# Kernel tuning notes

Measured on AMD Instinct MI355X. Metric: run time of the kernel, lower is better.

Reference implementation:

```python
import jax, jax.numpy as jnp
import numpy as np
import math

B, C, TC, H, W = 8, 256, 512, 48, 48
EPS = 1e-6

def setup_inputs() -> dict:
    key = jax.random.key(0)
    kx, kt, kq, kk, kv = jax.random.split(key, 5)
    x = jax.random.normal(kx, (B, C, H, W), dtype=jnp.float32)
    token = jax.random.normal(kt, (B, TC, H, W), dtype=jnp.float32)
    # xavier_uniform for 1x1 conv weights [out, in]
    def xavier(k, fan_out, fan_in):
        a = math.sqrt(6.0 / (fan_in + fan_out))
        return jax.random.uniform(k, (fan_out, fan_in), dtype=jnp.float32, minval=-a, maxval=a)
    Wq = xavier(kq, C, C)
    Wk = xavier(kk, C, TC)
    Wv = xavier(kv, C, TC)
    alpha = jnp.float32(0.5)  # nonzero so the attention path affects the output
    return {"x": x, "token": token, "Wq": Wq, "Wk": Wk, "Wv": Wv, "alpha": alpha}

def reference(x, token, Wq, Wk, Wv, alpha):
    # 1x1 convs == per-pixel GEMMs over the channel dim
    q = jnp.einsum('oc,bchw->bohw', Wq, x)       # [B,C,H,W]
    k = jnp.einsum('oc,bchw->bohw', Wk, token)   # [B,C,H,W]
    v = jnp.einsum('oc,bchw->bohw', Wv, token)   # [B,C,H,W]
    b, c, h, w = q.shape
    n = h * w
    qf = q.reshape(b, c, n).transpose(0, 2, 1)   # [B,N,C]
    kf = k.reshape(b, c, n)                      # [B,C,N]
    vf = v.reshape(b, c, n).transpose(0, 2, 1)   # [B,N,C]
    # cosine normalization over the channel dim (F.normalize with eps clamp)
    qn = qf / jnp.maximum(jnp.linalg.norm(qf, axis=-1, keepdims=True), EPS)
    kn = kf / jnp.maximum(jnp.linalg.norm(kf, axis=1, keepdims=True), EPS)
    attn = jnp.einsum('bnc,bcm->bnm', qn, kn) / math.sqrt(c)  # [B,N,N]
    attn = jax.nn.softmax(attn, axis=-1)
    out = jnp.einsum('bnm,bmc->bnc', attn, vf)   # [B,N,C]
    out = out.transpose(0, 2, 1).reshape(b, c, h, w)
    return x + alpha * out
```

## Files before the change

kernel.cpp:

```cpp
#include <hip/hip_runtime.h>

#define B_   8
#define C_   256
#define TC_  512
#define HW_  2304
#define EPS_ 1e-6f

typedef __bf16 bf16_t;
typedef __bf16 bf16x8 __attribute__((ext_vector_type(8)));
typedef __bf16 bf16x4_t __attribute__((ext_vector_type(4)));
typedef float  f32x4 __attribute__((ext_vector_type(4)));
typedef unsigned int  u32;
typedef long long     i64;
typedef unsigned char u8;

__device__ __forceinline__ void g2l16(const void* g, void* l) {
    __builtin_amdgcn_global_load_lds(
        (const __attribute__((address_space(1))) unsigned int*)g,
        (__attribute__((address_space(3))) unsigned int*)l, 16, 0, 0);
}

__device__ __forceinline__ u8 to_fp8(float v) {
    return (u8)(__builtin_amdgcn_cvt_pk_fp8_f32(v, v, 0, false) & 0xff);
}

__global__ __launch_bounds__(256)
void wfrag_kernel(const float* __restrict__ wq, const float* __restrict__ wk,
                  const float* __restrict__ wv,
                  bf16_t* __restrict__ oq, bf16_t* __restrict__ ok,
                  bf16_t* __restrict__ ov)
{
    const int fid = blockIdx.x * 4 + (threadIdx.x >> 6);
    const int lane = threadIdx.x & 63;
    const int l16 = lane & 15, quad = lane >> 4;

    const float* src; bf16_t* dst; int cin, f;
    if (fid < 128)      { src = wq; dst = oq; cin = C_;  f = fid; }
    else if (fid < 384) { src = wk; dst = ok; cin = TC_; f = fid - 128; }
    else                { src = wv; dst = ov; cin = TC_; f = fid - 384; }
    const int nks = cin / 32;
    const int ot = f / nks, ks = f % nks;

    const float* s = src + (size_t)(ot * 16 + l16) * cin + ks * 32 + quad * 8;
    float4 a = *(const float4*)(s);
    float4 b = *(const float4*)(s + 4);
    bf16x8 o;
    o[0] = (__bf16)a.x; o[1] = (__bf16)a.y; o[2] = (__bf16)a.z; o[3] = (__bf16)a.w;
    o[4] = (__bf16)b.x; o[5] = (__bf16)b.y; o[6] = (__bf16)b.z; o[7] = (__bf16)b.w;
    *(bf16x8*)(dst + (size_t)f * 512 + lane * 8) = o;
}

template<int CIN, bool DO_V, bool KFMT>
__global__ __launch_bounds__(256, 4)
void convqkv_kernel(const float* __restrict__ X, const bf16_t* __restrict__ Wa,
                    const bf16_t* __restrict__ Wvp, u8* __restrict__ outA,
                    u8* __restrict__ outV)
{
    const int bid = blockIdx.x;
    const int b  = bid & 7;
    const int n0 = (bid >> 3) * 16;
    const int tid = threadIdx.x;
    const int wv = tid >> 6;
    const int lane = tid & 63;
    const int quad = lane >> 4, l16 = lane & 15;
    const int NKS = CIN / 32;

    __shared__ bf16_t T[16][CIN + 8];
    __shared__ float ssp[4][16];

    {
        const float* Xb = X + (size_t)b * CIN * HW_ + n0;
        const int cl = tid >> 2;
        const int n4 = (tid & 3) * 4;
#pragma unroll
        for (int cp = 0; cp < CIN; cp += 64) {
            float4 v = *(const float4*)(Xb + (size_t)(cp + cl) * HW_ + n4);
            T[n4 + 0][cp + cl] = (__bf16)v.x;
            T[n4 + 1][cp + cl] = (__bf16)v.y;
            T[n4 + 2][cp + cl] = (__bf16)v.z;
            T[n4 + 3][cp + cl] = (__bf16)v.w;
        }
    }
    __syncthreads();

    bf16x8 af[CIN / 32];
#pragma unroll
    for (int ks = 0; ks < CIN / 32; ks++)
        af[ks] = *(const bf16x8*)(&T[l16][ks * 32 + quad * 8]);

    const int ot0 = wv * 4;

    f32x4 accK[4];
#pragma unroll
    for (int p = 0; p < 4; p++) accK[p] = (f32x4){0.f, 0.f, 0.f, 0.f};
    {
        const bf16_t* wbase = Wa + ((size_t)ot0 * NKS) * 512 + lane * 8;
#pragma unroll
        for (int ks = 0; ks < CIN / 32; ks++)
#pragma unroll
            for (int p = 0; p < 4; p++) {
                bf16x8 bw = *(const bf16x8*)(wbase + (size_t)(p * NKS + ks) * 512);
                accK[p] = __builtin_amdgcn_mfma_f32_16x16x32_bf16(af[ks], bw, accK[p], 0, 0, 0);
            }
    }

    {
        float ssr[4];
#pragma unroll
        for (int r = 0; r < 4; r++) {
            float ss = accK[0][r] * accK[0][r] + accK[1][r] * accK[1][r]
                     + accK[2][r] * accK[2][r] + accK[3][r] * accK[3][r];
            ss += __shfl_xor(ss, 1);
            ss += __shfl_xor(ss, 2);
            ss += __shfl_xor(ss, 4);
            ss += __shfl_xor(ss, 8);
            ssr[r] = ss;
        }
        if (l16 == 0) {
#pragma unroll
            for (int r = 0; r < 4; r++) ssp[wv][quad * 4 + r] = ssr[r];
        }
    }

    f32x4 accV[4];
    if (DO_V) {
#pragma unroll
        for (int p = 0; p < 4; p++) accV[p] = (f32x4){0.f, 0.f, 0.f, 0.f};
        const bf16_t* wbase = Wvp + ((size_t)ot0 * NKS) * 512 + lane * 8;
#pragma unroll
        for (int ks = 0; ks < CIN / 32; ks++)
#pragma unroll
            for (int p = 0; p < 4; p++) {
                bf16x8 aw = *(const bf16x8*)(wbase + (size_t)(p * NKS + ks) * 512);
                accV[p] = __builtin_amdgcn_mfma_f32_16x16x32_bf16(aw, af[ks], accV[p], 0, 0, 0);
            }
    }

    __syncthreads();

    float scale[4];
#pragma unroll
    for (int r = 0; r < 4; r++) {
        int px = quad * 4 + r;
        float s = ssp[0][px] + ssp[1][px] + ssp[2][px] + ssp[3][px];
        scale[r] = 1.0f / fmaxf(sqrtf(s), EPS_);
    }
    if (!KFMT) {
        u8* oa = outA + ((size_t)b * HW_ + n0 + quad * 4) * C_ + l16;
#pragma unroll
        for (int p = 0; p < 4; p++)
#pragma unroll
            for (int r = 0; r < 4; r++)
                oa[(size_t)r * C_ + (ot0 + p) * 16] = to_fp8(accK[p][r] * scale[r]);
    } else {
        u8* oa = outA + (size_t)b * 32 * HW_ * 8;
#pragma unroll
        for (int p = 0; p < 4; p++)
#pragma unroll
            for (int r = 0; r < 4; r++)
                oa[(((size_t)((ot0 + p) * 2 + (l16 >> 3))) * HW_
                    + n0 + quad * 4 + r) * 8 + (l16 & 7)]
                    = to_fp8(accK[p][r] * scale[r]);
    }

    if (DO_V) {
#pragma unroll
        for (int p = 0; p < 4; p++)
#pragma unroll
            for (int r = 0; r < 4; r++)
                outV[(((size_t)b * 288 + (n0 >> 3) + (l16 >> 3)) * 256
                      + (ot0 + p) * 16 + quad * 4 + r) * 8 + (l16 & 7)]
                    = to_fp8(accV[p][r]);
    }
}

__global__ __launch_bounds__(256, 3)
void attn_part_kernel(const u8* __restrict__ q8, const u8* __restrict__ k8,
                      const u8* __restrict__ v8,
                      bf16_t* __restrict__ Opart, float* __restrict__ lpart,
                      int tilesPerSplit, int JS)
{
    const int bid = blockIdx.x;
    const int b   = bid & 7;
    const int rr  = bid >> 3;
    const int js  = rr % JS;
    const int mt  = rr / JS;
    const int wv   = threadIdx.x >> 6;
    const int lane = threadIdx.x & 63;
    const int quad = lane >> 4;
    const int l16  = lane & 15;
    const int row0 = mt * 64 + wv * 16;
    const int jbase = js * tilesPerSplit * 32;

    const u8* qb = q8 + (size_t)b * HW_ * C_;
    const u8* kb = k8 + (size_t)b * 32 * HW_ * 8;
    const u8* vb = v8 + (size_t)b * 288 * 256 * 8;

    __shared__ u8 Kbuf[3][8192];
    __shared__ u8 Vbuf[3][8192];

    i64 aq[8];
    {
        const u8* r0 = qb + (size_t)(row0 + l16) * C_ + quad * 8;
#pragma unroll
        for (int t = 0; t < 8; t++) aq[t] = *(const i64*)(r0 + t * 32);
    }

    f32x4 O[16];
#pragma unroll
    for (int i = 0; i < 16; i++) O[i] = (f32x4){0.f, 0.f, 0.f, 0.f};
    float lsum = 0.f;

    const int sQuad = (lane >> 3) & 3;
    const int sRow2 = (lane & 7) * 2;
    const int sHi   = lane >> 5;

#define STAGE(bufi, j0g)                                                       \
    {                                                                          \
        _Pragma("unroll")                                                      \
        for (int p = 0; p < 2; p++) {                                          \
            int i = wv * 2 + p;                                                \
            g2l16(kb + ((size_t)(i * 4 + sQuad) * HW_                          \
                        + (j0g) + sRow2 + sHi * 16) * 8,                       \
                  &Kbuf[bufi][i * 1024]);                                      \
        }                                                                      \
        _Pragma("unroll")                                                      \
        for (int p = 0; p < 2; p++) {                                          \
            int i = wv * 2 + p;                                                \
            g2l16(vb + (((size_t)((j0g) >> 3) + sQuad) * 256                   \
                        + (2 * i + sHi) * 16 + sRow2) * 8,                     \
                  &Vbuf[bufi][i * 1024]);                                      \
        }                                                                      \
    }

    STAGE(0, jbase)
    STAGE(1, jbase + 32)

    const int roff = quad * 128 + l16 * 8;

    for (int tt = 0; tt < tilesPerSplit; tt++) {
        if (tt + 1 < tilesPerSplit) {
            asm volatile("s_waitcnt vmcnt(4)" ::: "memory");
        } else {
            asm volatile("s_waitcnt vmcnt(0)" ::: "memory");
        }
        __builtin_amdgcn_s_barrier();
        if (tt + 2 < tilesPerSplit)
            STAGE((tt + 2) % 3, jbase + (tt + 2) * 32)
        __builtin_amdgcn_sched_barrier(0);

        const u8* Kb = Kbuf[tt % 3];
        const u8* Vb = Vbuf[tt % 3];

        f32x4 s00 = (f32x4){0.f,0.f,0.f,0.f}, s01 = (f32x4){0.f,0.f,0.f,0.f};
        __builtin_amdgcn_s_setprio(1);
#pragma unroll
        for (int t = 0; t < 8; t++) {
            i64 bk0 = *(const i64*)(Kb + t * 1024 + roff);
            i64 bk1 = *(const i64*)(Kb + t * 1024 + roff + 512);
            s00 = __builtin_amdgcn_mfma_f32_16x16x32_fp8_fp8(bk0, aq[t], s00, 0, 0, 0);
            s01 = __builtin_amdgcn_mfma_f32_16x16x32_fp8_fp8(bk1, aq[t], s01, 0, 0, 0);
        }
        __builtin_amdgcn_s_setprio(0);

        float pA0 = __expf(s00[0] * 0.0625f), pA1 = __expf(s00[1] * 0.0625f);
        float pA2 = __expf(s00[2] * 0.0625f), pA3 = __expf(s00[3] * 0.0625f);
        float pB0 = __expf(s01[0] * 0.0625f), pB1 = __expf(s01[1] * 0.0625f);
        float pB2 = __expf(s01[2] * 0.0625f), pB3 = __expf(s01[3] * 0.0625f);
        lsum += (pA0 + pA1 + pA2 + pA3) + (pB0 + pB1 + pB2 + pB3);

        u32 A  = __builtin_amdgcn_cvt_pk_fp8_f32(pA0, pA1, 0, false);
        A      = __builtin_amdgcn_cvt_pk_fp8_f32(pA2, pA3, A, true);
        u32 Bw = __builtin_amdgcn_cvt_pk_fp8_f32(pB0, pB1, 0, false);
        Bw     = __builtin_amdgcn_cvt_pk_fp8_f32(pB2, pB3, Bw, true);

        asm volatile("v_permlane32_swap_b32 %0, %1" : "+v"(A), "+v"(Bw));
        asm volatile("v_permlane16_swap_b32 %0, %1" : "+v"(A), "+v"(Bw));
        i64 ap0 = ((i64)(u32)Bw << 32) | (i64)A;

        __builtin_amdgcn_s_setprio(1);
#pragma unroll
        for (int ct = 0; ct < 16; ct++) {
            i64 bv = *(const i64*)(Vb + ct * 512 + roff);
            O[ct] = __builtin_amdgcn_mfma_f32_16x16x32_fp8_fp8(ap0, bv, O[ct], 0, 0, 0);
        }
        __builtin_amdgcn_s_setprio(0);
    }

    lsum += __shfl_xor(lsum, 16);
    lsum += __shfl_xor(lsum, 32);
    float* lp = lpart + (size_t)(js * B_ + b) * HW_;
    if (quad == 0) lp[row0 + l16] = lsum;

    bf16_t* op = Opart + (size_t)(js * B_ + b) * C_ * HW_;
#pragma unroll
    for (int ct = 0; ct < 16; ct++) {
        int c = ct * 16 + l16;
        bf16x4_t v0;
        v0[0] = (__bf16)O[ct][0]; v0[1] = (__bf16)O[ct][1];
        v0[2] = (__bf16)O[ct][2]; v0[3] = (__bf16)O[ct][3];
        *(bf16x4_t*)(op + (size_t)c * HW_ + row0 + quad * 4) = v0;
    }
#undef STAGE
}

__global__ __launch_bounds__(256)
void epilogue_kernel(const float* __restrict__ x, const bf16_t* __restrict__ Opart,
                     const float* __restrict__ lpart, const float* __restrict__ alphaPtr,
                     float* __restrict__ out, int JS)
{
    const float a = *alphaPtr;
    const size_t S = (size_t)B_ * C_ * HW_;
    size_t flat = ((size_t)blockIdx.x * 256 + threadIdx.x) * 4;
    int bc = (int)(flat / HW_);
    int n  = (int)(flat % HW_);
    int b  = bc >> 8;
    float4 xv = *(const float4*)(x + flat);
    float s0 = 0.f, s1 = 0.f, s2 = 0.f, s3 = 0.f;
    float l0 = 0.f, l1 = 0.f, l2 = 0.f, l3 = 0.f;
    for (int js = 0; js < JS; js++) {
        bf16x4_t ov = *(const bf16x4_t*)(Opart + (size_t)js * S + flat);
        s0 += (float)ov[0]; s1 += (float)ov[1];
        s2 += (float)ov[2]; s3 += (float)ov[3];
        float4 lv = *(const float4*)(lpart + (size_t)(js * B_ + b) * HW_ + n);
        l0 += lv.x; l1 += lv.y; l2 += lv.z; l3 += lv.w;
    }
    float4 r;
    r.x = xv.x + a * s0 / l0;
    r.y = xv.y + a * s1 / l1;
    r.z = xv.z + a * s2 / l2;
    r.w = xv.w + a * s3 / l3;
    *(float4*)(out + flat) = r;
}

extern "C" void kernel_launch(void* const* d_in, const int* in_sizes, int n_in,
                              void* d_out, int out_size, void* d_ws, size_t ws_size,
                              hipStream_t stream)
{
    (void)in_sizes; (void)n_in; (void)out_size;
    const float* x     = (const float*)d_in[0];
    const float* token = (const float*)d_in[1];
    const float* Wq    = (const float*)d_in[2];
    const float* Wk    = (const float*)d_in[3];
    const float* Wv    = (const float*)d_in[4];
    const float* alpha = (const float*)d_in[5];
    float* out = (float*)d_out;

    const size_t S = (size_t)B_ * HW_ * C_;

    int JS = 4;
    for (;;) {
        size_t need = (12 + 2 * (size_t)JS) * S
                    + (size_t)JS * B_ * HW_ * 4 + (size_t)B_ * HW_ * 4;
        if (need <= ws_size || JS == 1) break;
        JS >>= 1;
    }
    const int tilesPerSplit = (HW_ / 32) / JS;

    char* ws = (char*)d_ws;
    bf16_t* WqL   = (bf16_t*)(ws + 6 * S);
    bf16_t* WkL   = WqL + (size_t)C_ * C_;
    bf16_t* WvL   = WkL + (size_t)C_ * TC_;
    u8*     q8    = (u8*)(ws + 7 * S);
    u8*     k8    = (u8*)(ws + 8 * S);
    u8*     v8    = (u8*)(ws + 9 * S);
    bf16_t* Opart = (bf16_t*)(ws + 12 * S);
    float*  lpart = (float*)(ws + (12 + 2 * (size_t)JS) * S);

    wfrag_kernel<<<dim3(160), dim3(256), 0, stream>>>(Wq, Wk, Wv, WqL, WkL, WvL);
    convqkv_kernel<C_,  false, false><<<dim3(B_ * HW_ / 16), dim3(256), 0, stream>>>(x,     WqL, nullptr, q8, nullptr);
    convqkv_kernel<TC_, true,  true ><<<dim3(B_ * HW_ / 16), dim3(256), 0, stream>>>(token, WkL, WvL,     k8, v8);
    attn_part_kernel<<<dim3(JS * B_ * (HW_ / 64)), dim3(256), 0, stream>>>(q8, k8, v8, Opart, lpart, tilesPerSplit, JS);
    epilogue_kernel<<<dim3((int)(S / 1024)), dim3(256), 0, stream>>>(x, Opart, lpart, alpha, out, JS);
}
```

Measured before the change: 220.1 us.

## Software-pipeline QK scores one tile ahead to overlap softmax exp with MFMA

Computes the QK^T score MFMAs for the next key tile before running exp/fp8 packing and PV MFMAs on the current tile. The aim is to hide the exp and conversion latency behind independent matrix work. Tile tt+1 must now be resident at the top of iteration tt, so the loop waits for all outstanding loads (vmcnt(0)). That shortens the effective prefetch distance and may expose more memory latency. It also adds register pressure for the extra score accumulators.

```diff
diff --git a/kernel.cpp b/kernel.cpp
--- a/kernel.cpp
+++ b/kernel.cpp
@@ -238,35 +238,50 @@
 
     const int roff = quad * 128 + l16 * 8;
 
+    f32x4 sA0, sA1;
+    {
+        asm volatile("s_waitcnt vmcnt(4)" ::: "memory");
+        __builtin_amdgcn_s_barrier();
+        __builtin_amdgcn_sched_barrier(0);
+        const u8* Kb = Kbuf[0];
+        f32x4 a0 = (f32x4){0.f,0.f,0.f,0.f}, a1 = (f32x4){0.f,0.f,0.f,0.f};
+        __builtin_amdgcn_s_setprio(1);
+#pragma unroll
+        for (int t = 0; t < 8; t++) {
+            i64 bk0 = *(const i64*)(Kb + t * 1024 + roff);
+            i64 bk1 = *(const i64*)(Kb + t * 1024 + roff + 512);
+            a0 = __builtin_amdgcn_mfma_f32_16x16x32_fp8_fp8(bk0, aq[t], a0, 0, 0, 0);
+            a1 = __builtin_amdgcn_mfma_f32_16x16x32_fp8_fp8(bk1, aq[t], a1, 0, 0, 0);
+        }
+        __builtin_amdgcn_s_setprio(0);
+        sA0 = a0; sA1 = a1;
+    }
+
     for (int tt = 0; tt < tilesPerSplit; tt++) {
-        if (tt + 1 < tilesPerSplit) {
-            asm volatile("s_waitcnt vmcnt(4)" ::: "memory");
-        } else {
-            asm volatile("s_waitcnt vmcnt(0)" ::: "memory");
-        }
+        asm volatile("s_waitcnt vmcnt(0)" ::: "memory");
         __builtin_amdgcn_s_barrier();
         if (tt + 2 < tilesPerSplit)
             STAGE((tt + 2) % 3, jbase + (tt + 2) * 32)
         __builtin_amdgcn_sched_barrier(0);
 
-        const u8* Kb = Kbuf[tt % 3];
-        const u8* Vb = Vbuf[tt % 3];
-
-        f32x4 s00 = (f32x4){0.f,0.f,0.f,0.f}, s01 = (f32x4){0.f,0.f,0.f,0.f};
-        __builtin_amdgcn_s_setprio(1);
-#pragma unroll
-        for (int t = 0; t < 8; t++) {
-            i64 bk0 = *(const i64*)(Kb + t * 1024 + roff);
-            i64 bk1 = *(const i64*)(Kb + t * 1024 + roff + 512);
-            s00 = __builtin_amdgcn_mfma_f32_16x16x32_fp8_fp8(bk0, aq[t], s00, 0, 0, 0);
-            s01 = __builtin_amdgcn_mfma_f32_16x16x32_fp8_fp8(bk1, aq[t], s01, 0, 0, 0);
-        }
-        __builtin_amdgcn_s_setprio(0);
-
-        float pA0 = __expf(s00[0] * 0.0625f), pA1 = __expf(s00[1] * 0.0625f);
-        float pA2 = __expf(s00[2] * 0.0625f), pA3 = __expf(s00[3] * 0.0625f);
-        float pB0 = __expf(s01[0] * 0.0625f), pB1 = __expf(s01[1] * 0.0625f);
-        float pB2 = __expf(s01[2] * 0.0625f), pB3 = __expf(s01[3] * 0.0625f);
+        f32x4 sB0 = (f32x4){0.f,0.f,0.f,0.f}, sB1 = (f32x4){0.f,0.f,0.f,0.f};
+        if (tt + 1 < tilesPerSplit) {
+            const u8* Kb = Kbuf[(tt + 1) % 3];
+            __builtin_amdgcn_s_setprio(1);
+#pragma unroll
+            for (int t = 0; t < 8; t++) {
+                i64 bk0 = *(const i64*)(Kb + t * 1024 + roff);
+                i64 bk1 = *(const i64*)(Kb + t * 1024 + roff + 512);
+                sB0 = __builtin_amdgcn_mfma_f32_16x16x32_fp8_fp8(bk0, aq[t], sB0, 0, 0, 0);
+                sB1 = __builtin_amdgcn_mfma_f32_16x16x32_fp8_fp8(bk1, aq[t], sB1, 0, 0, 0);
+            }
+            __builtin_amdgcn_s_setprio(0);
+        }
+
+        float pA0 = __expf(sA0[0] * 0.0625f), pA1 = __expf(sA0[1] * 0.0625f);
+        float pA2 = __expf(sA0[2] * 0.0625f), pA3 = __expf(sA0[3] * 0.0625f);
+        float pB0 = __expf(sA1[0] * 0.0625f), pB1 = __expf(sA1[1] * 0.0625f);
+        float pB2 = __expf(sA1[2] * 0.0625f), pB3 = __expf(sA1[3] * 0.0625f);
         lsum += (pA0 + pA1 + pA2 + pA3) + (pB0 + pB1 + pB2 + pB3);
 
         u32 A  = __builtin_amdgcn_cvt_pk_fp8_f32(pA0, pA1, 0, false);
@@ -278,6 +293,7 @@
         asm volatile("v_permlane16_swap_b32 %0, %1" : "+v"(A), "+v"(Bw));
         i64 ap0 = ((i64)(u32)Bw << 32) | (i64)A;
 
+        const u8* Vb = Vbuf[tt % 3];
         __builtin_amdgcn_s_setprio(1);
 #pragma unroll
         for (int ct = 0; ct < 16; ct++) {
@@ -285,6 +301,8 @@
             O[ct] = __builtin_amdgcn_mfma_f32_16x16x32_fp8_fp8(ap0, bv, O[ct], 0, 0, 0);
         }
         __builtin_amdgcn_s_setprio(0);
+
+        sA0 = sB0; sA1 = sB1;
     }
 
     lsum += __shfl_xor(lsum, 16);
```

Result: no change. 219.0 us (-0.5%).

## Widen conv QKV tiles to 64 pixels to reuse weight fragments across pixel groups

Applied to the files above, without the earlier changes.

The 1x1 conv projection kernel now processes 64 pixels per block instead of 16. Each weight fragment loaded from global memory feeds four MFMAs, one per 16-pixel group, which cuts weight traffic per pixel by four. The channel dimension is staged through LDS in 256-channel halves so the shared tile fits. The cost is a larger accumulator footprint (launch bounds drop to 2 waves per SIMD) and a quarter as many blocks, which may reduce occupancy and latency hiding.

```diff
diff --git a/kernel.cpp b/kernel.cpp
--- a/kernel.cpp
+++ b/kernel.cpp
@@ -51,126 +51,142 @@
 }
 
 template<int CIN, bool DO_V, bool KFMT>
-__global__ __launch_bounds__(256, 4)
+__global__ __launch_bounds__(256, 2)
 void convqkv_kernel(const float* __restrict__ X, const bf16_t* __restrict__ Wa,
                     const bf16_t* __restrict__ Wvp, u8* __restrict__ outA,
                     u8* __restrict__ outV)
 {
+    constexpr int HALVES = CIN / 256;
+    constexpr int NKS    = CIN / 32;
     const int bid = blockIdx.x;
     const int b  = bid & 7;
-    const int n0 = (bid >> 3) * 16;
+    const int n0 = (bid >> 3) * 64;
     const int tid = threadIdx.x;
     const int wv = tid >> 6;
     const int lane = tid & 63;
     const int quad = lane >> 4, l16 = lane & 15;
-    const int NKS = CIN / 32;
-
-    __shared__ bf16_t T[16][CIN + 8];
-    __shared__ float ssp[4][16];
-
-    {
-        const float* Xb = X + (size_t)b * CIN * HW_ + n0;
-        const int cl = tid >> 2;
-        const int n4 = (tid & 3) * 4;
-#pragma unroll
-        for (int cp = 0; cp < CIN; cp += 64) {
-            float4 v = *(const float4*)(Xb + (size_t)(cp + cl) * HW_ + n4);
-            T[n4 + 0][cp + cl] = (__bf16)v.x;
-            T[n4 + 1][cp + cl] = (__bf16)v.y;
-            T[n4 + 2][cp + cl] = (__bf16)v.z;
-            T[n4 + 3][cp + cl] = (__bf16)v.w;
-        }
-    }
-    __syncthreads();
-
-    bf16x8 af[CIN / 32];
-#pragma unroll
-    for (int ks = 0; ks < CIN / 32; ks++)
-        af[ks] = *(const bf16x8*)(&T[l16][ks * 32 + quad * 8]);
+
+    __shared__ bf16_t T[64][264];
+    __shared__ float ssp[4][64];
 
     const int ot0 = wv * 4;
 
-    f32x4 accK[4];
-#pragma unroll
-    for (int p = 0; p < 4; p++) accK[p] = (f32x4){0.f, 0.f, 0.f, 0.f};
-    {
-        const bf16_t* wbase = Wa + ((size_t)ot0 * NKS) * 512 + lane * 8;
-#pragma unroll
-        for (int ks = 0; ks < CIN / 32; ks++)
+    f32x4 accK[4][4];
+#pragma unroll
+    for (int g = 0; g < 4; g++)
+#pragma unroll
+        for (int p = 0; p < 4; p++) accK[g][p] = (f32x4){0.f, 0.f, 0.f, 0.f};
+    f32x4 accV[4][4];
+    if (DO_V) {
+#pragma unroll
+        for (int g = 0; g < 4; g++)
+#pragma unroll
+            for (int p = 0; p < 4; p++) accV[g][p] = (f32x4){0.f, 0.f, 0.f, 0.f};
+    }
+
+    const bf16_t* wkbase = Wa + (size_t)(ot0 * NKS) * 512 + lane * 8;
+    const bf16_t* wvbase = Wvp + (size_t)(ot0 * NKS) * 512 + lane * 8;
+
+#pragma unroll
+    for (int half = 0; half < HALVES; half++) {
+        {
+            const float* Xb = X + ((size_t)b * CIN + half * 256) * HW_ + n0;
+            const int cl = tid >> 4;
+            const int nn = (tid & 15) * 4;
+#pragma unroll
+            for (int cp = 0; cp < 256; cp += 16) {
+                float4 v = *(const float4*)(Xb + (size_t)(cp + cl) * HW_ + nn);
+                T[nn + 0][cp + cl] = (__bf16)v.x;
+                T[nn + 1][cp + cl] = (__bf16)v.y;
+                T[nn + 2][cp + cl] = (__bf16)v.z;
+                T[nn + 3][cp + cl] = (__bf16)v.w;
+            }
+        }
+        __syncthreads();
+
+#pragma unroll
+        for (int k8 = 0; k8 < 8; k8++) {
+            const int ks = half * 8 + k8;
+            bf16x8 af[4];
+#pragma unroll
+            for (int g = 0; g < 4; g++)
+                af[g] = *(const bf16x8*)(&T[g * 16 + l16][k8 * 32 + quad * 8]);
 #pragma unroll
             for (int p = 0; p < 4; p++) {
-                bf16x8 bw = *(const bf16x8*)(wbase + (size_t)(p * NKS + ks) * 512);
-                accK[p] = __builtin_amdgcn_mfma_f32_16x16x32_bf16(af[ks], bw, accK[p], 0, 0, 0);
+                bf16x8 bw = *(const bf16x8*)(wkbase + (size_t)(p * NKS + ks) * 512);
+#pragma unroll
+                for (int g = 0; g < 4; g++)
+                    accK[g][p] = __builtin_amdgcn_mfma_f32_16x16x32_bf16(af[g], bw, accK[g][p], 0, 0, 0);
             }
-    }
-
-    {
-        float ssr[4];
+            if (DO_V) {
+#pragma unroll
+                for (int p = 0; p < 4; p++) {
+                    bf16x8 aw = *(const bf16x8*)(wvbase + (size_t)(p * NKS + ks) * 512);
+#pragma unroll
+                    for (int g = 0; g < 4; g++)
+                        accV[g][p] = __builtin_amdgcn_mfma_f32_16x16x32_bf16(aw, af[g], accV[g][p], 0, 0, 0);
+                }
+            }
+        }
+        if (half + 1 < HALVES) __syncthreads();
+    }
+
+#pragma unroll
+    for (int g = 0; g < 4; g++)
 #pragma unroll
         for (int r = 0; r < 4; r++) {
-            float ss = accK[0][r] * accK[0][r] + accK[1][r] * accK[1][r]
-                     + accK[2][r] * accK[2][r] + accK[3][r] * accK[3][r];
+            float ss = accK[g][0][r] * accK[g][0][r] + accK[g][1][r] * accK[g][1][r]
+                     + accK[g][2][r] * accK[g][2][r] + accK[g][3][r] * accK[g][3][r];
             ss += __shfl_xor(ss, 1);
             ss += __shfl_xor(ss, 2);
             ss += __shfl_xor(ss, 4);
             ss += __shfl_xor(ss, 8);
-            ssr[r] = ss;
-        }
-        if (l16 == 0) {
-#pragma unroll
-            for (int r = 0; r < 4; r++) ssp[wv][quad * 4 + r] = ssr[r];
-        }
-    }
-
-    f32x4 accV[4];
-    if (DO_V) {
-#pragma unroll
-        for (int p = 0; p < 4; p++) accV[p] = (f32x4){0.f, 0.f, 0.f, 0.f};
-        const bf16_t* wbase = Wvp + ((size_t)ot0 * NKS) * 512 + lane * 8;
-#pragma unroll
-        for (int ks = 0; ks < CIN / 32; ks++)
-#pragma unroll
-            for (int p = 0; p < 4; p++) {
-                bf16x8 aw = *(const bf16x8*)(wbase + (size_t)(p * NKS + ks) * 512);
-                accV[p] = __builtin_amdgcn_mfma_f32_16x16x32_bf16(aw, af[ks], accV[p], 0, 0, 0);
-            }
-    }
-
+            if (l16 == 0) ssp[wv][g * 16 + quad * 4 + r] = ss;
+        }
     __syncthreads();
 
-    float scale[4];
-#pragma unroll
-    for (int r = 0; r < 4; r++) {
-        int px = quad * 4 + r;
-        float s = ssp[0][px] + ssp[1][px] + ssp[2][px] + ssp[3][px];
-        scale[r] = 1.0f / fmaxf(sqrtf(s), EPS_);
-    }
+    float scale[4][4];
+#pragma unroll
+    for (int g = 0; g < 4; g++)
+#pragma unroll
+        for (int r = 0; r < 4; r++) {
+            int px = g * 16 + quad * 4 + r;
+            float s = ssp[0][px] + ssp[1][px] + ssp[2][px] + ssp[3][px];
+            scale[g][r] = 1.0f / fmaxf(sqrtf(s), EPS_);
+        }
+
     if (!KFMT) {
-        u8* oa = outA + ((size_t)b * HW_ + n0 + quad * 4) * C_ + l16;
-#pragma unroll
-        for (int p = 0; p < 4; p++)
-#pragma unroll
-            for (int r = 0; r < 4; r++)
-                oa[(size_t)r * C_ + (ot0 + p) * 16] = to_fp8(accK[p][r] * scale[r]);
+        u8* oa = outA + ((size_t)b * HW_ + n0) * C_;
+#pragma unroll
+        for (int g = 0; g < 4; g++)
+#pragma unroll
+            for (int p = 0; p < 4; p++)
+#pragma unroll
+                for (int r = 0; r < 4; r++)
+                    oa[(size_t)(g * 16 + quad * 4 + r) * C_ + (ot0 + p) * 16 + l16]
+                        = to_fp8(accK[g][p][r] * scale[g][r]);
     } else {
         u8* oa = outA + (size_t)b * 32 * HW_ * 8;
 #pragma unroll
-        for (int p = 0; p < 4; p++)
-#pragma unroll
-            for (int r = 0; r < 4; r++)
-                oa[(((size_t)((ot0 + p) * 2 + (l16 >> 3))) * HW_
-                    + n0 + quad * 4 + r) * 8 + (l16 & 7)]
-                    = to_fp8(accK[p][r] * scale[r]);
-    }
-
+        for (int g = 0; g < 4; g++)
+#pragma unroll
+            for (int p = 0; p < 4; p++)
+#pragma unroll
+                for (int r = 0; r < 4; r++)
+                    oa[((size_t)((ot0 + p) * 2 + (l16 >> 3)) * HW_
+                        + n0 + g * 16 + quad * 4 + r) * 8 + (l16 & 7)]
+                        = to_fp8(accK[g][p][r] * scale[g][r]);
+    }
     if (DO_V) {
 #pragma unroll
-        for (int p = 0; p < 4; p++)
-#pragma unroll
-            for (int r = 0; r < 4; r++)
-                outV[(((size_t)b * 288 + (n0 >> 3) + (l16 >> 3)) * 256
-                      + (ot0 + p) * 16 + quad * 4 + r) * 8 + (l16 & 7)]
-                    = to_fp8(accV[p][r]);
+        for (int g = 0; g < 4; g++)
+#pragma unroll
+            for (int p = 0; p < 4; p++)
+#pragma unroll
+                for (int r = 0; r < 4; r++)
+                    outV[(((size_t)b * 288 + (n0 >> 3) + g * 2 + (l16 >> 3)) * 256
+                          + (ot0 + p) * 16 + quad * 4 + r) * 8 + (l16 & 7)]
+                        = to_fp8(accV[g][p][r]);
     }
 }
 
@@ -368,8 +384,8 @@
     float*  lpart = (float*)(ws + (12 + 2 * (size_t)JS) * S);
 
     wfrag_kernel<<<dim3(160), dim3(256), 0, stream>>>(Wq, Wk, Wv, WqL, WkL, WvL);
-    convqkv_kernel<C_,  false, false><<<dim3(B_ * HW_ / 16), dim3(256), 0, stream>>>(x,     WqL, nullptr, q8, nullptr);
-    convqkv_kernel<TC_, true,  true ><<<dim3(B_ * HW_ / 16), dim3(256), 0, stream>>>(token, WkL, WvL,     k8, v8);
+    convqkv_kernel<C_,  false, false><<<dim3(B_ * HW_ / 64), dim3(256), 0, stream>>>(x,     WqL, nullptr, q8, nullptr);
+    convqkv_kernel<TC_, true,  true ><<<dim3(B_ * HW_ / 64), dim3(256), 0, stream>>>(token, WkL, WvL,     k8, v8);
     attn_part_kernel<<<dim3(JS * B_ * (HW_ / 64)), dim3(256), 0, stream>>>(q8, k8, v8, Opart, lpart, tilesPerSplit, JS);
     epilogue_kernel<<<dim3((int)(S / 1024)), dim3(256), 0, stream>>>(x, Opart, lpart, alpha, out, JS);
 }
```

New measurement: 231.1 us. 1.05x slower.

## Drop split-K attention and fuse normalization epilogue; merge Q and KV conv launches

Applied to the files above, without the earlier changes.

The attention kernel no longer splits the key dimension into JS partitions. Each block now walks all key tiles and applies the softmax normalization, the alpha scaling and the residual add directly from registers. This removes the bf16 partial-output and partial-sum buffers and the separate epilogue kernel. The Q and K/V projection kernels are also merged into one launch that dispatches on block index and uses shared memory sized for the larger case. The cost is that the attention grid shrinks fourfold, to 288 blocks with four times the serial work per block, which leaves many compute units with a single block or none and reduces latency hiding.

```diff
diff --git a/kernel.cpp b/kernel.cpp
--- a/kernel.cpp
+++ b/kernel.cpp
@@ -8,7 +8,6 @@
 
 typedef __bf16 bf16_t;
 typedef __bf16 bf16x8 __attribute__((ext_vector_type(8)));
-typedef __bf16 bf16x4_t __attribute__((ext_vector_type(4)));
 typedef float  f32x4 __attribute__((ext_vector_type(4)));
 typedef unsigned int  u32;
 typedef long long     i64;
@@ -51,12 +50,12 @@
 }
 
 template<int CIN, bool DO_V, bool KFMT>
-__global__ __launch_bounds__(256, 4)
-void convqkv_kernel(const float* __restrict__ X, const bf16_t* __restrict__ Wa,
-                    const bf16_t* __restrict__ Wvp, u8* __restrict__ outA,
-                    u8* __restrict__ outV)
-{
-    const int bid = blockIdx.x;
+__device__ __forceinline__ void conv_body(const float* __restrict__ X,
+                                          const bf16_t* __restrict__ Wa,
+                                          const bf16_t* __restrict__ Wvp,
+                                          u8* __restrict__ outA, u8* __restrict__ outV,
+                                          int bid, u8* smem)
+{
     const int b  = bid & 7;
     const int n0 = (bid >> 3) * 16;
     const int tid = threadIdx.x;
@@ -65,8 +64,8 @@
     const int quad = lane >> 4, l16 = lane & 15;
     const int NKS = CIN / 32;
 
-    __shared__ bf16_t T[16][CIN + 8];
-    __shared__ float ssp[4][16];
+    bf16_t (*T)[CIN + 8] = (bf16_t (*)[CIN + 8])smem;
+    float (*ssp)[16] = (float (*)[16])(smem + (size_t)16 * (CIN + 8) * 2);
 
     {
         const float* Xb = X + (size_t)b * CIN * HW_ + n0;
@@ -174,23 +173,34 @@
     }
 }
 
+__global__ __launch_bounds__(256, 4)
+void convqkv_kernel(const float* __restrict__ x, const float* __restrict__ token,
+                    const bf16_t* __restrict__ WqL, const bf16_t* __restrict__ WkL,
+                    const bf16_t* __restrict__ WvL,
+                    u8* __restrict__ q8, u8* __restrict__ k8, u8* __restrict__ v8)
+{
+    __shared__ __align__(16) u8 smem[16 * (TC_ + 8) * 2 + 256];
+    const int NB1 = B_ * HW_ / 16;
+    if ((int)blockIdx.x < NB1)
+        conv_body<C_,  false, false>(x,     WqL, nullptr, q8, nullptr, blockIdx.x, smem);
+    else
+        conv_body<TC_, true,  true >(token, WkL, WvL,     k8, v8, blockIdx.x - NB1, smem);
+}
+
 __global__ __launch_bounds__(256, 3)
-void attn_part_kernel(const u8* __restrict__ q8, const u8* __restrict__ k8,
-                      const u8* __restrict__ v8,
-                      bf16_t* __restrict__ Opart, float* __restrict__ lpart,
-                      int tilesPerSplit, int JS)
+void attn_final_kernel(const u8* __restrict__ q8, const u8* __restrict__ k8,
+                       const u8* __restrict__ v8, const float* __restrict__ x,
+                       const float* __restrict__ alphaPtr, float* __restrict__ out)
 {
     const int bid = blockIdx.x;
     const int b   = bid & 7;
-    const int rr  = bid >> 3;
-    const int js  = rr % JS;
-    const int mt  = rr / JS;
+    const int mt  = bid >> 3;
     const int wv   = threadIdx.x >> 6;
     const int lane = threadIdx.x & 63;
     const int quad = lane >> 4;
     const int l16  = lane & 15;
     const int row0 = mt * 64 + wv * 16;
-    const int jbase = js * tilesPerSplit * 32;
+    const int NT = HW_ / 32;
 
     const u8* qb = q8 + (size_t)b * HW_ * C_;
     const u8* kb = k8 + (size_t)b * 32 * HW_ * 8;
@@ -198,6 +208,7 @@
 
     __shared__ u8 Kbuf[3][8192];
     __shared__ u8 Vbuf[3][8192];
+    __shared__ float lsb[4][16];
 
     i64 aq[8];
     {
@@ -233,20 +244,20 @@
         }                                                                      \
     }
 
-    STAGE(0, jbase)
-    STAGE(1, jbase + 32)
+    STAGE(0, 0)
+    STAGE(1, 32)
 
     const int roff = quad * 128 + l16 * 8;
 
-    for (int tt = 0; tt < tilesPerSplit; tt++) {
-        if (tt + 1 < tilesPerSplit) {
+    for (int tt = 0; tt < NT; tt++) {
+        if (tt + 1 < NT) {
             asm volatile("s_waitcnt vmcnt(4)" ::: "memory");
         } else {
             asm volatile("s_waitcnt vmcnt(0)" ::: "memory");
         }
         __builtin_amdgcn_s_barrier();
-        if (tt + 2 < tilesPerSplit)
-            STAGE((tt + 2) % 3, jbase + (tt + 2) * 32)
+        if (tt + 2 < NT)
+            STAGE((tt + 2) % 3, (tt + 2) * 32)
         __builtin_amdgcn_sched_barrier(0);
 
         const u8* Kb = Kbuf[tt % 3];
@@ -289,55 +300,33 @@
 
     lsum += __shfl_xor(lsum, 16);
     lsum += __shfl_xor(lsum, 32);
-    float* lp = lpart + (size_t)(js * B_ + b) * HW_;
-    if (quad == 0) lp[row0 + l16] = lsum;
-
-    bf16_t* op = Opart + (size_t)(js * B_ + b) * C_ * HW_;
+    if (quad == 0) lsb[wv][l16] = lsum;
+    __syncthreads();
+
+    const float a = *alphaPtr;
+    float inv[4];
+#pragma unroll
+    for (int r = 0; r < 4; r++) inv[r] = a / lsb[wv][quad * 4 + r];
+
+    const float* xb = x   + (size_t)b * C_ * HW_;
+    float*       ob = out + (size_t)b * C_ * HW_;
 #pragma unroll
     for (int ct = 0; ct < 16; ct++) {
         int c = ct * 16 + l16;
-        bf16x4_t v0;
-        v0[0] = (__bf16)O[ct][0]; v0[1] = (__bf16)O[ct][1];
-        v0[2] = (__bf16)O[ct][2]; v0[3] = (__bf16)O[ct][3];
-        *(bf16x4_t*)(op + (size_t)c * HW_ + row0 + quad * 4) = v0;
+        f32x4 xv = *(const f32x4*)(xb + (size_t)c * HW_ + row0 + quad * 4);
+        f32x4 rv;
+#pragma unroll
+        for (int r = 0; r < 4; r++) rv[r] = xv[r] + O[ct][r] * inv[r];
+        *(f32x4*)(ob + (size_t)c * HW_ + row0 + quad * 4) = rv;
     }
 #undef STAGE
-}
-
-__global__ __launch_bounds__(256)
-void epilogue_kernel(const float* __restrict__ x, const bf16_t* __restrict__ Opart,
-                     const float* __restrict__ lpart, const float* __restrict__ alphaPtr,
-                     float* __restrict__ out, int JS)
-{
-    const float a = *alphaPtr;
-    const size_t S = (size_t)B_ * C_ * HW_;
-    size_t flat = ((size_t)blockIdx.x * 256 + threadIdx.x) * 4;
-    int bc = (int)(flat / HW_);
-    int n  = (int)(flat % HW_);
-    int b  = bc >> 8;
-    float4 xv = *(const float4*)(x + flat);
-    float s0 = 0.f, s1 = 0.f, s2 = 0.f, s3 = 0.f;
-    float l0 = 0.f, l1 = 0.f, l2 = 0.f, l3 = 0.f;
-    for (int js = 0; js < JS; js++) {
-        bf16x4_t ov = *(const bf16x4_t*)(Opart + (size_t)js * S + flat);
-        s0 += (float)ov[0]; s1 += (float)ov[1];
-        s2 += (float)ov[2]; s3 += (float)ov[3];
-        float4 lv = *(const float4*)(lpart + (size_t)(js * B_ + b) * HW_ + n);
-        l0 += lv.x; l1 += lv.y; l2 += lv.z; l3 += lv.w;
-    }
-    float4 r;
-    r.x = xv.x + a * s0 / l0;
-    r.y = xv.y + a * s1 / l1;
-    r.z = xv.z + a * s2 / l2;
-    r.w = xv.w + a * s3 / l3;
-    *(float4*)(out + flat) = r;
 }
 
 extern "C" void kernel_launch(void* const* d_in, const int* in_sizes, int n_in,
                               void* d_out, int out_size, void* d_ws, size_t ws_size,
                               hipStream_t stream)
 {
-    (void)in_sizes; (void)n_in; (void)out_size;
+    (void)in_sizes; (void)n_in; (void)out_size; (void)ws_size;
     const float* x     = (const float*)d_in[0];
     const float* token = (const float*)d_in[1];
     const float* Wq    = (const float*)d_in[2];
@@ -348,28 +337,15 @@
 
     const size_t S = (size_t)B_ * HW_ * C_;
 
-    int JS = 4;
-    for (;;) {
-        size_t need = (12 + 2 * (size_t)JS) * S
-                    + (size_t)JS * B_ * HW_ * 4 + (size_t)B_ * HW_ * 4;
-        if (need <= ws_size || JS == 1) break;
-        JS >>= 1;
-    }
-    const int tilesPerSplit = (HW_ / 32) / JS;
-
     char* ws = (char*)d_ws;
-    bf16_t* WqL   = (bf16_t*)(ws + 6 * S);
-    bf16_t* WkL   = WqL + (size_t)C_ * C_;
-    bf16_t* WvL   = WkL + (size_t)C_ * TC_;
-    u8*     q8    = (u8*)(ws + 7 * S);
-    u8*     k8    = (u8*)(ws + 8 * S);
-    u8*     v8    = (u8*)(ws + 9 * S);
-    bf16_t* Opart = (bf16_t*)(ws + 12 * S);
-    float*  lpart = (float*)(ws + (12 + 2 * (size_t)JS) * S);
+    bf16_t* WqL = (bf16_t*)(ws + 6 * S);
+    bf16_t* WkL = WqL + (size_t)C_ * C_;
+    bf16_t* WvL = WkL + (size_t)C_ * TC_;
+    u8*     q8  = (u8*)(ws + 7 * S);
+    u8*     k8  = (u8*)(ws + 8 * S);
+    u8*     v8  = (u8*)(ws + 9 * S);
 
     wfrag_kernel<<<dim3(160), dim3(256), 0, stream>>>(Wq, Wk, Wv, WqL, WkL, WvL);
-    convqkv_kernel<C_,  false, false><<<dim3(B_ * HW_ / 16), dim3(256), 0, stream>>>(x,     WqL, nullptr, q8, nullptr);
-    convqkv_kernel<TC_, true,  true ><<<dim3(B_ * HW_ / 16), dim3(256), 0, stream>>>(token, WkL, WvL,     k8, v8);
-    attn_part_kernel<<<dim3(JS * B_ * (HW_ / 64)), dim3(256), 0, stream>>>(q8, k8, v8, Opart, lpart, tilesPerSplit, JS);
-    epilogue_kernel<<<dim3((int)(S / 1024)), dim3(256), 0, stream>>>(x, Opart, lpart, alpha, out, JS);
-}
+    convqkv_kernel<<<dim3(2 * B_ * HW_ / 16), dim3(256), 0, stream>>>(x, token, WqL, WkL, WvL, q8, k8, v8);
+    attn_final_kernel<<<dim3(B_ * (HW_ / 64)), dim3(256), 0, stream>>>(q8, k8, v8, x, alpha, out);
+}
```

Measured after the change: 233.2 us. +6.0%, slower.
